# Kernel tuning notes

Hardware: AMD Instinct MI355X
Metric: run time of the kernel (lower is better)

## Reference

```python
import jax, jax.numpy as jnp
import numpy as np

B, D_IN, D, H, HD, M = 4096, 512, 128, 8, 16, 128
L = M + 1            # 1 query token + M memory slots
D_FF = 512
SCALE = 0.25         # 1/sqrt(HD)


def _ln(x, w, b, eps=1e-5):
    m = jnp.mean(x, axis=-1, keepdims=True)
    v = jnp.var(x, axis=-1, keepdims=True)
    return (x - m) * jax.lax.rsqrt(v + eps) * w + b


def setup_inputs() -> dict:
    ks = jax.random.split(jax.random.key(0), 26)
    n = lambda i, shape, s=1.0: jax.random.normal(ks[i], shape, jnp.float32) * s
    return {
        "x": n(0, (B, 1, D_IN)),
        "W_in": n(1, (D, D_IN), 0.05),
        "b_in": n(2, (D,), 0.02),
        "pos": n(3, (B, 1, D), 0.02),
        "mask": jnp.zeros((B, M), jnp.float32),  # additive attention bias for memory slots
        "mem": n(5, (B, M, D)),
        "ln1_w": jnp.ones((D,), jnp.float32), "ln1_b": jnp.zeros((D,), jnp.float32),
        "W_qkv": n(8, (3 * D, D), 0.09),
        "b_qkv": n(9, (3 * D,), 0.02),
        "W_out": n(10, (D, D), 0.09),
        "b_out": n(11, (D,), 0.02),
        "ln2_w": jnp.ones((D,), jnp.float32), "ln2_b": jnp.zeros((D,), jnp.float32),
        "ln3_w": jnp.ones((D,), jnp.float32), "ln3_b": jnp.zeros((D,), jnp.float32),
        "W_ff1": n(16, (D_FF, D), 0.09),
        "b_ff1": n(17, (D_FF,), 0.02),
        "ln4_w": jnp.ones((D_FF,), jnp.float32), "ln4_b": jnp.zeros((D_FF,), jnp.float32),
        "W_ff2": n(20, (D, D_FF), 0.04),
        "b_ff2": n(21, (D,), 0.02),
        "ln5_w": jnp.ones((D,), jnp.float32), "ln5_b": jnp.zeros((D,), jnp.float32),
        "W_head": n(24, (D_IN, D), 0.09),
        "b_head": n(25, (D_IN,), 0.02),
    }


def reference(x, W_in, b_in, pos, mask, mem, ln1_w, ln1_b, W_qkv, b_qkv,
              W_out, b_out, ln2_w, ln2_b, ln3_w, ln3_b, W_ff1, b_ff1,
              ln4_w, ln4_b, W_ff2, b_ff2, ln5_w, ln5_b, W_head, b_head):
    Bn = x.shape[0]
    # input projection + positional offset -> single query token per row  [B,1,D]
    q_in = (x.reshape(Bn, D_IN) @ W_in.T + b_in)[:, None, :] + pos
    # additive attention bias: 0 for the query slot, `mask` for memory slots  [B,L]
    bias = jnp.concatenate([jnp.zeros((Bn, 1), x.dtype), mask], axis=1)
    kv_in = jnp.concatenate([q_in, mem], axis=1)           # [B,L,D]
    kv_ln = _ln(kv_in, ln1_w, ln1_b)
    Wq, Wkv = W_qkv[:D], W_qkv[D:]
    bq, bkv = b_qkv[:D], b_qkv[D:]
    q = q_in[:, 0] @ Wq.T + bq                             # [B,D]  (Q uses UN-normalized q_in)
    kv = kv_ln @ Wkv.T + bkv                               # [B,L,2D]
    k, v = kv[..., :D], kv[..., D:]
    qh = q.reshape(Bn, H, HD)
    kh = k.reshape(Bn, L, H, HD)
    vh = v.reshape(Bn, L, H, HD)
    scores = jnp.einsum('bhd,blhd->bhl', qh * SCALE, kh) + bias[:, None, :]
    p = jax.nn.softmax(scores, axis=-1)                    # [B,H,L]
    o = jnp.einsum('bhl,blhd->bhd', p, vh).reshape(Bn, D)
    attn = _ln((o @ W_out.T + b_out)[:, None, :], ln2_w, ln2_b)
    h = attn + q_in                                        # residual  [B,1,D]
    f = _ln(h, ln3_w, ln3_b) @ W_ff1.T + b_ff1             # [B,1,D_FF]
    f = 0.5 * f * (1.0 + jax.lax.erf(f * 0.7071067811865476))  # exact GELU
    f = _ln(f, ln4_w, ln4_b) @ W_ff2.T + b_ff2             # [B,1,D]
    h2 = _ln(f + h, ln5_w, ln5_b)
    return h2 @ W_head.T + b_head                          # [B,1,D_IN]
```

## Files before the change

### kernel.cpp

```cpp
#include <hip/hip_runtime.h>

namespace {

constexpr int Dn   = 128;
constexpr int DIN  = 512;
constexpr int Hn   = 8;
constexpr int Mn   = 128;
constexpr int DFF  = 512;
constexpr int GA   = 4;
constexpr int GC   = 8;
constexpr float ATT_SCALE = 0.25f;
constexpr float INV_SQRT2 = 0.70710678118654752440f;

typedef short  short8v  __attribute__((ext_vector_type(8)));
typedef float  float4v  __attribute__((ext_vector_type(4)));

__device__ __forceinline__ unsigned pk_bf16(float lo, float hi) {
    unsigned r;
    asm volatile("v_cvt_pk_bf16_f32 %0, %1, %2" : "=v"(r) : "v"(lo), "v"(hi));
    return r;
}
__device__ __forceinline__ float lo16(unsigned u) { return __uint_as_float(u << 16); }
__device__ __forceinline__ float hi16(unsigned u) { return __uint_as_float(u & 0xffff0000u); }

__device__ __forceinline__ float dot128(const float* __restrict__ wrow,
                                        const float* __restrict__ v)
{
    const float4* w4 = (const float4*)wrow;
    const float4* v4 = (const float4*)v;
    float acc = 0.f;
#pragma unroll
    for (int j = 0; j < 32; ++j) {
        float4 a = w4[j], b = v4[j];
        acc += a.x*b.x + a.y*b.y + a.z*b.z + a.w*b.w;
    }
    return acc;
}

template <int NCOL>
__device__ __forceinline__ void ln_row64(const float* __restrict__ src,
                                         float* __restrict__ dst,
                                         const float* __restrict__ gw,
                                         const float* __restrict__ gb,
                                         const float* __restrict__ resid,
                                         int sub)
{
    constexpr int E = NCOL / 64;
    float v0[E]; float sm = 0.f;
#pragma unroll
    for (int i = 0; i < E; ++i) { v0[i] = src[sub*E + i]; sm += v0[i]; }
#pragma unroll
    for (int m = 32; m >= 1; m >>= 1) sm += __shfl_xor(sm, m);
    float mean = sm * (1.f / (float)NCOL);
    float vs = 0.f;
#pragma unroll
    for (int i = 0; i < E; ++i) { float d0 = v0[i] - mean; vs += d0*d0; }
#pragma unroll
    for (int m = 32; m >= 1; m >>= 1) vs += __shfl_xor(vs, m);
    float rstd = rsqrtf(vs * (1.f / (float)NCOL) + 1e-5f);
#pragma unroll
    for (int i = 0; i < E; ++i) {
        int d = sub*E + i;
        float r = (v0[i] - mean) * rstd * gw[d] + gb[d];
        dst[d] = resid ? (r + resid[d]) : r;
    }
}

__global__ __launch_bounds__(256, 2)
void k_qin(const float* __restrict__ x, const float* __restrict__ W_in,
           const float* __restrict__ b_in, const float* __restrict__ pos,
           float* __restrict__ q_in)
{
    const int t  = threadIdx.x;
    const int b0 = blockIdx.x * 8;
    __shared__ __align__(16) float s_x[8 * DIN];
    {
        const float4* src = (const float4*)(x + (size_t)b0 * DIN);
        float4* dst = (float4*)s_x;
#pragma unroll
        for (int i = 0; i < 4; ++i) dst[t + 256*i] = src[t + 256*i];
    }
    __syncthreads();
    {
        int d = t & 127, gq = t >> 7;
        const float4* w4 = (const float4*)(W_in + (size_t)d * DIN);
        float acc[4] = {0,0,0,0};
        for (int j = 0; j < DIN/4; ++j) {
            float4 a = w4[j];
#pragma unroll
            for (int g = 0; g < 4; ++g) {
                float4 xv = ((const float4*)s_x)[(gq*4 + g)*(DIN/4) + j];
                acc[g] = fmaf(a.x, xv.x, acc[g]); acc[g] = fmaf(a.y, xv.y, acc[g]);
                acc[g] = fmaf(a.z, xv.z, acc[g]); acc[g] = fmaf(a.w, xv.w, acc[g]);
            }
        }
#pragma unroll
        for (int g = 0; g < 4; ++g) {
            int gb = b0 + gq*4 + g;
            q_in[(size_t)gb*Dn + d] = acc[g] + b_in[d] + pos[(size_t)gb*Dn + d];
        }
    }
}

__global__ __launch_bounds__(256, 2)
void k_attn(const float* __restrict__ q_in,
            const float* __restrict__ mask,
            const float* __restrict__ mem,
            const float* __restrict__ ln1_w, const float* __restrict__ ln1_b,
            const float* __restrict__ W_qkv, const float* __restrict__ b_qkv,
            float* __restrict__ o_ws)
{
    const int t    = threadIdx.x;
    const int lane = t & 63;
    const int wv   = t >> 6;
    const int b0   = blockIdx.x * GA;

    __shared__ __align__(16) unsigned short s16[2][Mn * Dn];
    __shared__ __align__(16) float s_X[1312];
    __shared__ __align__(16) float s_lnq[Dn];
    __shared__ __align__(16) float s_q[Dn];
    __shared__ __align__(16) float s_qin[GA][Dn];
    __shared__ float s_s2c[Hn], s_s0[Hn], s_den[Hn], s_p0[Hn];

    unsigned short* s_At = (unsigned short*)s_X;
    float* s_sc = s_X;

    float4 pr[16];
    {
        const float4* src = (const float4*)(mem + (size_t)b0 * Mn * Dn);
#pragma unroll
        for (int i = 0; i < 16; ++i) pr[i] = src[t + 256*i];
    }
    if (t < 128)
        ((float4*)&s_qin[0][0])[t] = ((const float4*)(q_in + (size_t)b0*Dn))[t];
    __syncthreads();

    for (int g = 0; g < GA; ++g) {
        const int p = g & 1;

#pragma unroll
        for (int i = 0; i < 16; ++i) {
            int fid = t + 256*i;
            int r = fid >> 5, k = fid & 31;
            int c = k >> 1, half = k & 1;
            unsigned u0 = pk_bf16(pr[i].x, pr[i].y), u1 = pk_bf16(pr[i].z, pr[i].w);
            *(uint2*)&s16[p][r*128 + ((c ^ (r & 7)) << 3) + half*4] = make_uint2(u0, u1);
        }
        if (g + 1 < GA) {
            const float4* src = (const float4*)(mem + (size_t)(b0+g+1) * Mn * Dn);
#pragma unroll
            for (int i = 0; i < 16; ++i) pr[i] = src[t + 256*i];
        }
        if (t < 64) {
            ln_row64<Dn>(&s_qin[g][0], s_lnq, ln1_w, ln1_b, nullptr, t);
        } else if (t >= 128) {
            int dd = t - 128;
            s_q[dd] = dot128(W_qkv + (size_t)dd*Dn, &s_qin[g][0]) + b_qkv[dd];
        }
        __syncthreads();

        {
            int h = t >> 5, js = t & 31;
            float aq[4] = {0,0,0,0};
            float ch = 0.f;
#pragma unroll
            for (int d0 = 0; d0 < 16; ++d0) {
                float qv = s_q[h*16 + d0];
                float4 w = ((const float4*)(W_qkv + (size_t)(Dn + h*16 + d0)*Dn))[js];
                aq[0] = fmaf(qv, w.x, aq[0]); aq[1] = fmaf(qv, w.y, aq[1]);
                aq[2] = fmaf(qv, w.z, aq[2]); aq[3] = fmaf(qv, w.w, aq[3]);
                ch = fmaf(qv, b_qkv[Dn + h*16 + d0], ch);
            }
            ch *= ATT_SCALE;
            float s1p = 0.f, s2p = 0.f, s0p = 0.f;
            float aqw[4];
#pragma unroll
            for (int c = 0; c < 4; ++c) {
                int j = js*4 + c;
                float a = ATT_SCALE * aq[c];
                aqw[c] = a * ln1_w[j];
                s1p += aqw[c];
                s2p = fmaf(a, ln1_b[j], s2p);
                s0p = fmaf(a, s_lnq[j], s0p);
            }
#pragma unroll
            for (int m = 16; m >= 1; m >>= 1) {
                s1p += __shfl_xor(s1p, m, 32);
                s2p += __shfl_xor(s2p, m, 32);
                s0p += __shfl_xor(s0p, m, 32);
            }
            float sub = s1p * (1.f/128.f);
            *(unsigned*)&s_At[h*136 + 4*js]     = pk_bf16(aqw[0]-sub, aqw[1]-sub);
            *(unsigned*)&s_At[h*136 + 4*js + 2] = pk_bf16(aqw[2]-sub, aqw[3]-sub);
            if (js == 0) { s_s2c[h] = s2p + ch; s_s0[h] = s0p + ch; }
            unsigned* X32 = (unsigned*)s_At;
            for (int idx = t; idx < 544; idx += 256) X32[8*68 + idx] = 0;
        }
        __syncthreads();

        float4v acc0 = {0.f,0.f,0.f,0.f}, acc1 = {0.f,0.f,0.f,0.f};
        float rstd_reg = 0.f;
        {
            const int al = lane & 15, ag = lane >> 4;
            const int r0 = (2*wv)*16 + al, r1 = (2*wv+1)*16 + al;
#pragma unroll
            for (int ks = 0; ks < 4; ++ks) {
                short8v af = *(const short8v*)&s_At[al*136 + ks*32 + ag*8];
                int c = ks*4 + ag;
                short8v f0 = *(const short8v*)&s16[p][r0*128 + ((c ^ (r0 & 7)) << 3)];
                short8v f1 = *(const short8v*)&s16[p][r1*128 + ((c ^ (r1 & 7)) << 3)];
                acc0 = __builtin_amdgcn_mfma_f32_16x16x32_bf16(af, f0, acc0, 0, 0, 0);
                acc1 = __builtin_amdgcn_mfma_f32_16x16x32_bf16(af, f1, acc1, 0, 0, 0);
            }
            int r = t >> 1, hf = t & 1;
            float sum = 0.f, ssq = 0.f;
#pragma unroll
            for (int kk = 0; kk < 8; ++kk) {
                int c = hf*8 + kk;
                uint4 tv = *(const uint4*)&s16[p][r*128 + ((c ^ (r & 7)) << 3)];
                float vv[8];
                vv[0] = lo16(tv.x); vv[1] = hi16(tv.x);
                vv[2] = lo16(tv.y); vv[3] = hi16(tv.y);
                vv[4] = lo16(tv.z); vv[5] = hi16(tv.z);
                vv[6] = lo16(tv.w); vv[7] = hi16(tv.w);
#pragma unroll
                for (int q = 0; q < 8; ++q) { sum += vv[q]; ssq = fmaf(vv[q], vv[q], ssq); }
            }
            sum += __shfl_xor(sum, 1);
            ssq += __shfl_xor(ssq, 1);
            float mean = sum * (1.f/128.f);
            float var  = fmaf(-mean, mean, ssq * (1.f/128.f));
            rstd_reg = rsqrtf(var + 1e-5f);
        }
        __syncthreads();

        {
            if (lane < 32) {
                int al = lane & 15, hb = (lane >> 4) * 4;
                int r0 = (2*wv)*16 + al, r1 = (2*wv+1)*16 + al;
#pragma unroll
                for (int reg = 0; reg < 4; ++reg) {
                    s_sc[r0*10 + hb + reg] = acc0[reg];
                    s_sc[r1*10 + hb + reg] = acc1[reg];
                }
            }
            if ((t & 1) == 0) s_sc[(t >> 1)*10 + 8] = rstd_reg;
        }
        __syncthreads();

        {
            int w = wv, l = lane;
            int h0 = 2*w, h1 = h0 + 1;
            int r0 = 2*l, r1 = r0 + 1;
            float2 da = *(const float2*)&s_sc[r0*10 + h0];
            float2 db = *(const float2*)&s_sc[r1*10 + h0];
            float rs0 = s_sc[r0*10 + 8], rs1 = s_sc[r1*10 + 8];
            float2 mk = *(const float2*)&mask[(size_t)(b0+g)*Mn + r0];
            float sc00 = fmaf(rs0, da.x, s_s2c[h0]) + mk.x;
            float sc01 = fmaf(rs0, da.y, s_s2c[h1]) + mk.x;
            float sc10 = fmaf(rs1, db.x, s_s2c[h0]) + mk.y;
            float sc11 = fmaf(rs1, db.y, s_s2c[h1]) + mk.y;
            float mx0 = fmaxf(sc00, sc10), mx1 = fmaxf(sc01, sc11);
#pragma unroll
            for (int m = 1; m < 64; m <<= 1) {
                mx0 = fmaxf(mx0, __shfl_xor(mx0, m));
                mx1 = fmaxf(mx1, __shfl_xor(mx1, m));
            }
            mx0 = fmaxf(mx0, s_s0[h0]);
            mx1 = fmaxf(mx1, s_s0[h1]);
            float e00 = __expf(sc00 - mx0), e10 = __expf(sc10 - mx0);
            float e01 = __expf(sc01 - mx1), e11 = __expf(sc11 - mx1);
            float ds0 = e00 + e10, ds1 = e01 + e11;
#pragma unroll
            for (int m = 1; m < 64; m <<= 1) {
                ds0 += __shfl_xor(ds0, m);
                ds1 += __shfl_xor(ds1, m);
            }
            float p00 = __expf(s_s0[h0] - mx0), p01 = __expf(s_s0[h1] - mx1);
            *(float2*)&s_sc[r0*10 + h0] = make_float2(e00*rs0, e01*rs0);
            *(float2*)&s_sc[r1*10 + h0] = make_float2(e10*rs1, e11*rs1);
            if (l == 0) {
                s_den[h0] = ds0 + p00; s_p0[h0] = p00;
                s_den[h1] = ds1 + p01; s_p0[h1] = p01;
            }
        }
        __syncthreads();

        float cx0[8], cx1[8], cS0, cS1;
        {
            int w = wv, l = lane;
            int qtr = l >> 4, c = l & 15;
#pragma unroll
            for (int q = 0; q < 8; ++q) { cx0[q] = 0.f; cx1[q] = 0.f; }
#pragma unroll 4
            for (int rr = 0; rr < 32; ++rr) {
                int r = qtr*32 + rr;
                uint4 tv = *(const uint4*)&s16[p][r*128 + ((c ^ (r & 7)) << 3)];
                float2 qv = *(const float2*)&s_sc[r*10 + 2*w];
                float v0 = lo16(tv.x), v1 = hi16(tv.x);
                float v2 = lo16(tv.y), v3 = hi16(tv.y);
                float v4 = lo16(tv.z), v5 = hi16(tv.z);
                float v6 = lo16(tv.w), v7 = hi16(tv.w);
                cx0[0]=fmaf(qv.x,v0,cx0[0]); cx1[0]=fmaf(qv.y,v0,cx1[0]);
                cx0[1]=fmaf(qv.x,v1,cx0[1]); cx1[1]=fmaf(qv.y,v1,cx1[1]);
                cx0[2]=fmaf(qv.x,v2,cx0[2]); cx1[2]=fmaf(qv.y,v2,cx1[2]);
                cx0[3]=fmaf(qv.x,v3,cx0[3]); cx1[3]=fmaf(qv.y,v3,cx1[3]);
                cx0[4]=fmaf(qv.x,v4,cx0[4]); cx1[4]=fmaf(qv.y,v4,cx1[4]);
                cx0[5]=fmaf(qv.x,v5,cx0[5]); cx1[5]=fmaf(qv.y,v5,cx1[5]);
                cx0[6]=fmaf(qv.x,v6,cx0[6]); cx1[6]=fmaf(qv.y,v6,cx1[6]);
                cx0[7]=fmaf(qv.x,v7,cx0[7]); cx1[7]=fmaf(qv.y,v7,cx1[7]);
            }
#pragma unroll
            for (int q = 0; q < 8; ++q) {
                cx0[q] += __shfl_xor(cx0[q], 16);
                cx0[q] += __shfl_xor(cx0[q], 32);
                cx1[q] += __shfl_xor(cx1[q], 16);
                cx1[q] += __shfl_xor(cx1[q], 32);
            }
            float sA = ((cx0[0]+cx0[1])+(cx0[2]+cx0[3])) + ((cx0[4]+cx0[5])+(cx0[6]+cx0[7]));
            float sB = ((cx1[0]+cx1[1])+(cx1[2]+cx1[3])) + ((cx1[4]+cx1[5])+(cx1[6]+cx1[7]));
#pragma unroll
            for (int m = 1; m < 16; m <<= 1) {
                sA += __shfl_xor(sA, m);
                sB += __shfl_xor(sB, m);
            }
            cS0 = sA * (1.f/128.f);
            cS1 = sB * (1.f/128.f);
        }
        __syncthreads();

        if (lane < 16) {
            int c = lane;
            int h0 = 2*wv, h1 = h0 + 1;
            float den0 = s_den[h0], p0a = s_p0[h0], sP0 = den0 - p0a, inv0 = 1.f/den0;
            float den1 = s_den[h1], p0b = s_p0[h1], sP1 = den1 - p0b, inv1 = 1.f/den1;
#pragma unroll
            for (int q = 0; q < 2; ++q) {
                int j0 = c*8 + q*4;
                float4 lq = *(const float4*)&s_lnq[j0];
                float4 lw = *(const float4*)&ln1_w[j0];
                float4 lb = *(const float4*)&ln1_b[j0];
                float4 o0, o1;
                o0.x = (p0a*lq.x + lw.x*(cx0[q*4+0]-cS0) + lb.x*sP0) * inv0;
                o0.y = (p0a*lq.y + lw.y*(cx0[q*4+1]-cS0) + lb.y*sP0) * inv0;
                o0.z = (p0a*lq.z + lw.z*(cx0[q*4+2]-cS0) + lb.z*sP0) * inv0;
                o0.w = (p0a*lq.w + lw.w*(cx0[q*4+3]-cS0) + lb.w*sP0) * inv0;
                o1.x = (p0b*lq.x + lw.x*(cx1[q*4+0]-cS1) + lb.x*sP1) * inv1;
                o1.y = (p0b*lq.y + lw.y*(cx1[q*4+1]-cS1) + lb.y*sP1) * inv1;
                o1.z = (p0b*lq.z + lw.z*(cx1[q*4+2]-cS1) + lb.z*sP1) * inv1;
                o1.w = (p0b*lq.w + lw.w*(cx1[q*4+3]-cS1) + lb.w*sP1) * inv1;
                *(float4*)&s_X[h0*128 + j0] = o0;
                *(float4*)&s_X[h1*128 + j0] = o1;
            }
        }
        __syncthreads();

        {
            int d = t >> 1, half = t & 1;
            int h = d >> 4;
            const float4* w4 = (const float4*)(W_qkv + (size_t)(2*Dn + d)*Dn) + half*16;
            const float4* c4 = (const float4*)&s_X[h*128] + half*16;
            float acc = 0.f;
#pragma unroll
            for (int j = 0; j < 16; ++j) {
                float4 a = w4[j], v = c4[j];
                acc += a.x*v.x + a.y*v.y + a.z*v.z + a.w*v.w;
            }
            acc += __shfl_xor(acc, 1);
            if (half == 0)
                o_ws[(size_t)(b0+g)*Dn + d] = acc + b_qkv[2*Dn + d];
        }
        __syncthreads();
    }
}

__global__ __launch_bounds__(256, 2)
void k_tail(const float* __restrict__ q_in, const float* __restrict__ o_ws,
            const float* __restrict__ W_out, const float* __restrict__ b_out,
            const float* __restrict__ ln2_w, const float* __restrict__ ln2_b,
            const float* __restrict__ ln3_w, const float* __restrict__ ln3_b,
            const float* __restrict__ W_ff1, const float* __restrict__ b_ff1,
            const float* __restrict__ ln4_w, const float* __restrict__ ln4_b,
            const float* __restrict__ W_ff2, const float* __restrict__ b_ff2,
            const float* __restrict__ ln5_w, const float* __restrict__ ln5_b,
            const float* __restrict__ W_head, const float* __restrict__ b_head,
            float* __restrict__ out)
{
    const int t    = threadIdx.x;
    const int lane = t & 63;
    const int wv   = t >> 6;
    const int b0   = blockIdx.x * GC;

    __shared__ __align__(16) float s_qi[GC][Dn];
    __shared__ __align__(16) float s_o [GC][Dn];
    __shared__ __align__(16) float s_t1[GC][Dn];
    __shared__ __align__(16) float s_h [GC][Dn];
    __shared__ __align__(16) float s_l3[GC][Dn];
    __shared__ __align__(16) float s_f1[GC * DFF];

    ((float4*)&s_qi[0][0])[t] = ((const float4*)(q_in + (size_t)b0*Dn))[t];
    ((float4*)&s_o [0][0])[t] = ((const float4*)(o_ws + (size_t)b0*Dn))[t];
    __syncthreads();

    {
        int d = t & 127, grp = t >> 7;
        const float4* w4 = (const float4*)(W_out + (size_t)d * Dn);
        float acc[4] = {0,0,0,0};
#pragma unroll 8
        for (int j = 0; j < 32; ++j) {
            float4 a = w4[j];
#pragma unroll
            for (int gg = 0; gg < 4; ++gg) {
                float4 v = *(const float4*)&s_o[grp*4 + gg][j*4];
                acc[gg] = fmaf(a.x,v.x,acc[gg]); acc[gg] = fmaf(a.y,v.y,acc[gg]);
                acc[gg] = fmaf(a.z,v.z,acc[gg]); acc[gg] = fmaf(a.w,v.w,acc[gg]);
            }
        }
#pragma unroll
        for (int gg = 0; gg < 4; ++gg) s_t1[grp*4 + gg][d] = acc[gg] + b_out[d];
    }
    __syncthreads();

    ln_row64<Dn>(&s_t1[wv][0], &s_h[wv][0], ln2_w, ln2_b, &s_qi[wv][0], lane);
    ln_row64<Dn>(&s_t1[wv+4][0], &s_h[wv+4][0], ln2_w, ln2_b, &s_qi[wv+4][0], lane);
    __syncthreads();
    ln_row64<Dn>(&s_h[wv][0], &s_l3[wv][0], ln3_w, ln3_b, nullptr, lane);
    ln_row64<Dn>(&s_h[wv+4][0], &s_l3[wv+4][0], ln3_w, ln3_b, nullptr, lane);
    __syncthreads();

    {
        int e0 = t, e1 = t + 256;
        const float4* wa = (const float4*)(W_ff1 + (size_t)e0 * Dn);
        const float4* wb = (const float4*)(W_ff1 + (size_t)e1 * Dn);
        float acc0[GC], acc1[GC];
#pragma unroll
        for (int g = 0; g < GC; ++g) { acc0[g] = 0.f; acc1[g] = 0.f; }
#pragma unroll 2
        for (int j = 0; j < 32; ++j) {
            float4 a = wa[j], bb = wb[j];
#pragma unroll
            for (int g = 0; g < GC; ++g) {
                float4 v = *(const float4*)&s_l3[g][j*4];
                acc0[g] = fmaf(a.x,v.x,acc0[g]);  acc0[g] = fmaf(a.y,v.y,acc0[g]);
                acc0[g] = fmaf(a.z,v.z,acc0[g]);  acc0[g] = fmaf(a.w,v.w,acc0[g]);
                acc1[g] = fmaf(bb.x,v.x,acc1[g]); acc1[g] = fmaf(bb.y,v.y,acc1[g]);
                acc1[g] = fmaf(bb.z,v.z,acc1[g]); acc1[g] = fmaf(bb.w,v.w,acc1[g]);
            }
        }
#pragma unroll
        for (int g = 0; g < GC; ++g) {
            float v0 = acc0[g] + b_ff1[e0];
            float v1 = acc1[g] + b_ff1[e1];
            s_f1[g*DFF + e0] = 0.5f * v0 * (1.f + erff(v0 * INV_SQRT2));
            s_f1[g*DFF + e1] = 0.5f * v1 * (1.f + erff(v1 * INV_SQRT2));
        }
    }
    __syncthreads();

    ln_row64<DFF>(&s_f1[wv*DFF], &s_f1[wv*DFF], ln4_w, ln4_b, nullptr, lane);
    ln_row64<DFF>(&s_f1[(wv+4)*DFF], &s_f1[(wv+4)*DFF], ln4_w, ln4_b, nullptr, lane);
    __syncthreads();

    {
        int d = t & 127, grp = t >> 7;
        const float4* w4 = (const float4*)(W_ff2 + (size_t)d * DFF);
        float acc[4] = {0,0,0,0};
#pragma unroll 4
        for (int j = 0; j < DFF/4; ++j) {
            float4 a = w4[j];
#pragma unroll
            for (int gg = 0; gg < 4; ++gg) {
                float4 v = ((const float4*)&s_f1[(grp*4 + gg)*DFF])[j];
                acc[gg] = fmaf(a.x,v.x,acc[gg]); acc[gg] = fmaf(a.y,v.y,acc[gg]);
                acc[gg] = fmaf(a.z,v.z,acc[gg]); acc[gg] = fmaf(a.w,v.w,acc[gg]);
            }
        }
#pragma unroll
        for (int gg = 0; gg < 4; ++gg)
            s_t1[grp*4 + gg][d] = acc[gg] + b_ff2[d] + s_h[grp*4 + gg][d];
    }
    __syncthreads();

    ln_row64<Dn>(&s_t1[wv][0], &s_o[wv][0], ln5_w, ln5_b, nullptr, lane);
    ln_row64<Dn>(&s_t1[wv+4][0], &s_o[wv+4][0], ln5_w, ln5_b, nullptr, lane);
    __syncthreads();

    {
        int e0 = t, e1 = t + 256;
        const float4* wa = (const float4*)(W_head + (size_t)e0 * Dn);
        const float4* wb = (const float4*)(W_head + (size_t)e1 * Dn);
        float acc0[GC], acc1[GC];
#pragma unroll
        for (int g = 0; g < GC; ++g) { acc0[g] = 0.f; acc1[g] = 0.f; }
#pragma unroll 2
        for (int j = 0; j < 32; ++j) {
            float4 a = wa[j], bb = wb[j];
#pragma unroll
            for (int g = 0; g < GC; ++g) {
                float4 v = *(const float4*)&s_o[g][j*4];
                acc0[g] = fmaf(a.x,v.x,acc0[g]);  acc0[g] = fmaf(a.y,v.y,acc0[g]);
                acc0[g] = fmaf(a.z,v.z,acc0[g]);  acc0[g] = fmaf(a.w,v.w,acc0[g]);
                acc1[g] = fmaf(bb.x,v.x,acc1[g]); acc1[g] = fmaf(bb.y,v.y,acc1[g]);
                acc1[g] = fmaf(bb.z,v.z,acc1[g]); acc1[g] = fmaf(bb.w,v.w,acc1[g]);
            }
        }
#pragma unroll
        for (int g = 0; g < GC; ++g) {
            out[(size_t)(b0+g)*DIN + e0] = acc0[g] + b_head[e0];
            out[(size_t)(b0+g)*DIN + e1] = acc1[g] + b_head[e1];
        }
    }
}

}

extern "C" void kernel_launch(void* const* d_in, const int* in_sizes, int n_in,
                              void* d_out, int out_size, void* d_ws, size_t ws_size,
                              hipStream_t stream)
{
    const float* x      = (const float*)d_in[0];
    const float* W_in   = (const float*)d_in[1];
    const float* b_in   = (const float*)d_in[2];
    const float* pos    = (const float*)d_in[3];
    const float* mask   = (const float*)d_in[4];
    const float* mem    = (const float*)d_in[5];
    const float* ln1_w  = (const float*)d_in[6];
    const float* ln1_b  = (const float*)d_in[7];
    const float* W_qkv  = (const float*)d_in[8];
    const float* b_qkv  = (const float*)d_in[9];
    const float* W_out  = (const float*)d_in[10];
    const float* b_out  = (const float*)d_in[11];
    const float* ln2_w  = (const float*)d_in[12];
    const float* ln2_b  = (const float*)d_in[13];
    const float* ln3_w  = (const float*)d_in[14];
    const float* ln3_b  = (const float*)d_in[15];
    const float* W_ff1  = (const float*)d_in[16];
    const float* b_ff1  = (const float*)d_in[17];
    const float* ln4_w  = (const float*)d_in[18];
    const float* ln4_b  = (const float*)d_in[19];
    const float* W_ff2  = (const float*)d_in[20];
    const float* b_ff2  = (const float*)d_in[21];
    const float* ln5_w  = (const float*)d_in[22];
    const float* ln5_b  = (const float*)d_in[23];
    const float* W_head = (const float*)d_in[24];
    const float* b_head = (const float*)d_in[25];

    const int B = in_sizes[0] / DIN;
    float* ws_qin = (float*)d_ws;
    float* ws_o   = (float*)d_ws + (size_t)B * Dn;

    k_qin<<<dim3(B / 8), dim3(256), 0, stream>>>(x, W_in, b_in, pos, ws_qin);
    k_attn<<<dim3(B / GA), dim3(256), 0, stream>>>(ws_qin, mask, mem,
                                                   ln1_w, ln1_b, W_qkv, b_qkv, ws_o);
    k_tail<<<dim3(B / GC), dim3(256), 0, stream>>>(ws_qin, ws_o,
        W_out, b_out, ln2_w, ln2_b, ln3_w, ln3_b,
        W_ff1, b_ff1, ln4_w, ln4_b, W_ff2, b_ff2,
        ln5_w, ln5_b, W_head, b_head, (float*)d_out);
}
```

Baseline: 268.5 us.

## Process one batch row per attention block instead of register-prefetched groups of four

The attention kernel now launches one block per batch row rather than looping over four rows per block with a register prefetch of the next row's memory tile and double-buffered bf16 shared memory. This halves shared memory per block and frees the 64 prefetch registers, so more blocks can be resident and the hardware overlaps memory loads across blocks instead of within one. In exchange, each block loses software pipelining and re-reads the W_qkv weights for every row, and launches four times as many blocks.

Measured after the change: 254.3 us. -5.3%, faster.

```diff
diff --git a/kernel.cpp b/kernel.cpp
--- a/kernel.cpp
+++ b/kernel.cpp
@@ -7,7 +7,6 @@
 constexpr int Hn   = 8;
 constexpr int Mn   = 128;
 constexpr int DFF  = 512;
-constexpr int GA   = 4;
 constexpr int GC   = 8;
 constexpr float ATT_SCALE = 0.25f;
 constexpr float INV_SQRT2 = 0.70710678118654752440f;
@@ -113,264 +112,251 @@
     const int t    = threadIdx.x;
     const int lane = t & 63;
     const int wv   = t >> 6;
-    const int b0   = blockIdx.x * GA;
-
-    __shared__ __align__(16) unsigned short s16[2][Mn * Dn];
+    const int b    = blockIdx.x;
+
+    __shared__ __align__(16) unsigned short s16[Mn * Dn];
     __shared__ __align__(16) float s_X[1312];
     __shared__ __align__(16) float s_lnq[Dn];
+    __shared__ __align__(16) float s_qi[Dn];
     __shared__ __align__(16) float s_q[Dn];
-    __shared__ __align__(16) float s_qin[GA][Dn];
     __shared__ float s_s2c[Hn], s_s0[Hn], s_den[Hn], s_p0[Hn];
 
     unsigned short* s_At = (unsigned short*)s_X;
     float* s_sc = s_X;
 
-    float4 pr[16];
-    {
-        const float4* src = (const float4*)(mem + (size_t)b0 * Mn * Dn);
-#pragma unroll
-        for (int i = 0; i < 16; ++i) pr[i] = src[t + 256*i];
-    }
-    if (t < 128)
-        ((float4*)&s_qin[0][0])[t] = ((const float4*)(q_in + (size_t)b0*Dn))[t];
-    __syncthreads();
-
-    for (int g = 0; g < GA; ++g) {
-        const int p = g & 1;
-
+    if (t < 32) ((float4*)s_qi)[t] = ((const float4*)(q_in + (size_t)b*Dn))[t];
+    __syncthreads();
+
+    {
+        const float4* src = (const float4*)(mem + (size_t)b * Mn * Dn);
 #pragma unroll
         for (int i = 0; i < 16; ++i) {
             int fid = t + 256*i;
+            float4 v = src[fid];
             int r = fid >> 5, k = fid & 31;
             int c = k >> 1, half = k & 1;
-            unsigned u0 = pk_bf16(pr[i].x, pr[i].y), u1 = pk_bf16(pr[i].z, pr[i].w);
-            *(uint2*)&s16[p][r*128 + ((c ^ (r & 7)) << 3) + half*4] = make_uint2(u0, u1);
-        }
-        if (g + 1 < GA) {
-            const float4* src = (const float4*)(mem + (size_t)(b0+g+1) * Mn * Dn);
-#pragma unroll
-            for (int i = 0; i < 16; ++i) pr[i] = src[t + 256*i];
-        }
-        if (t < 64) {
-            ln_row64<Dn>(&s_qin[g][0], s_lnq, ln1_w, ln1_b, nullptr, t);
-        } else if (t >= 128) {
-            int dd = t - 128;
-            s_q[dd] = dot128(W_qkv + (size_t)dd*Dn, &s_qin[g][0]) + b_qkv[dd];
-        }
-        __syncthreads();
-
-        {
-            int h = t >> 5, js = t & 31;
-            float aq[4] = {0,0,0,0};
-            float ch = 0.f;
-#pragma unroll
-            for (int d0 = 0; d0 < 16; ++d0) {
-                float qv = s_q[h*16 + d0];
-                float4 w = ((const float4*)(W_qkv + (size_t)(Dn + h*16 + d0)*Dn))[js];
-                aq[0] = fmaf(qv, w.x, aq[0]); aq[1] = fmaf(qv, w.y, aq[1]);
-                aq[2] = fmaf(qv, w.z, aq[2]); aq[3] = fmaf(qv, w.w, aq[3]);
-                ch = fmaf(qv, b_qkv[Dn + h*16 + d0], ch);
+            unsigned u0 = pk_bf16(v.x, v.y), u1 = pk_bf16(v.z, v.w);
+            *(uint2*)&s16[r*128 + ((c ^ (r & 7)) << 3) + half*4] = make_uint2(u0, u1);
+        }
+    }
+    if (t < 64) {
+        ln_row64<Dn>(s_qi, s_lnq, ln1_w, ln1_b, nullptr, t);
+    } else if (t >= 128) {
+        int dd = t - 128;
+        s_q[dd] = dot128(W_qkv + (size_t)dd*Dn, s_qi) + b_qkv[dd];
+    }
+    __syncthreads();
+
+    {
+        int h = t >> 5, js = t & 31;
+        float aq[4] = {0,0,0,0};
+        float ch = 0.f;
+#pragma unroll
+        for (int d0 = 0; d0 < 16; ++d0) {
+            float qv = s_q[h*16 + d0];
+            float4 w = ((const float4*)(W_qkv + (size_t)(Dn + h*16 + d0)*Dn))[js];
+            aq[0] = fmaf(qv, w.x, aq[0]); aq[1] = fmaf(qv, w.y, aq[1]);
+            aq[2] = fmaf(qv, w.z, aq[2]); aq[3] = fmaf(qv, w.w, aq[3]);
+            ch = fmaf(qv, b_qkv[Dn + h*16 + d0], ch);
+        }
+        ch *= ATT_SCALE;
+        float s1p = 0.f, s2p = 0.f, s0p = 0.f;
+        float aqw[4];
+#pragma unroll
+        for (int c = 0; c < 4; ++c) {
+            int j = js*4 + c;
+            float a = ATT_SCALE * aq[c];
+            aqw[c] = a * ln1_w[j];
+            s1p += aqw[c];
+            s2p = fmaf(a, ln1_b[j], s2p);
+            s0p = fmaf(a, s_lnq[j], s0p);
+        }
+#pragma unroll
+        for (int m = 16; m >= 1; m >>= 1) {
+            s1p += __shfl_xor(s1p, m, 32);
+            s2p += __shfl_xor(s2p, m, 32);
+            s0p += __shfl_xor(s0p, m, 32);
+        }
+        float sub = s1p * (1.f/128.f);
+        *(unsigned*)&s_At[h*136 + 4*js]     = pk_bf16(aqw[0]-sub, aqw[1]-sub);
+        *(unsigned*)&s_At[h*136 + 4*js + 2] = pk_bf16(aqw[2]-sub, aqw[3]-sub);
+        if (js == 0) { s_s2c[h] = s2p + ch; s_s0[h] = s0p + ch; }
+        unsigned* X32 = (unsigned*)s_At;
+        for (int idx = t; idx < 544; idx += 256) X32[8*68 + idx] = 0;
+    }
+    __syncthreads();
+
+    float4v acc0 = {0.f,0.f,0.f,0.f}, acc1 = {0.f,0.f,0.f,0.f};
+    float rstd_reg = 0.f;
+    {
+        const int al = lane & 15, ag = lane >> 4;
+        const int r0 = (2*wv)*16 + al, r1 = (2*wv+1)*16 + al;
+#pragma unroll
+        for (int ks = 0; ks < 4; ++ks) {
+            short8v af = *(const short8v*)&s_At[al*136 + ks*32 + ag*8];
+            int c = ks*4 + ag;
+            short8v b0 = *(const short8v*)&s16[r0*128 + ((c ^ (r0 & 7)) << 3)];
+            short8v b1 = *(const short8v*)&s16[r1*128 + ((c ^ (r1 & 7)) << 3)];
+            acc0 = __builtin_amdgcn_mfma_f32_16x16x32_bf16(af, b0, acc0, 0, 0, 0);
+            acc1 = __builtin_amdgcn_mfma_f32_16x16x32_bf16(af, b1, acc1, 0, 0, 0);
+        }
+        int r = t >> 1, hf = t & 1;
+        float sum = 0.f, ssq = 0.f;
+#pragma unroll
+        for (int kk = 0; kk < 8; ++kk) {
+            int c = hf*8 + kk;
+            uint4 tv = *(const uint4*)&s16[r*128 + ((c ^ (r & 7)) << 3)];
+            float vv[8];
+            vv[0] = lo16(tv.x); vv[1] = hi16(tv.x);
+            vv[2] = lo16(tv.y); vv[3] = hi16(tv.y);
+            vv[4] = lo16(tv.z); vv[5] = hi16(tv.z);
+            vv[6] = lo16(tv.w); vv[7] = hi16(tv.w);
+#pragma unroll
+            for (int q = 0; q < 8; ++q) { sum += vv[q]; ssq = fmaf(vv[q], vv[q], ssq); }
+        }
+        sum += __shfl_xor(sum, 1);
+        ssq += __shfl_xor(ssq, 1);
+        float mean = sum * (1.f/128.f);
+        float var  = fmaf(-mean, mean, ssq * (1.f/128.f));
+        rstd_reg = rsqrtf(var + 1e-5f);
+    }
+    __syncthreads();
+
+    {
+        if (lane < 32) {
+            int al = lane & 15, hb = (lane >> 4) * 4;
+            int r0 = (2*wv)*16 + al, r1 = (2*wv+1)*16 + al;
+#pragma unroll
+            for (int reg = 0; reg < 4; ++reg) {
+                s_sc[r0*10 + hb + reg] = acc0[reg];
+                s_sc[r1*10 + hb + reg] = acc1[reg];
             }
-            ch *= ATT_SCALE;
-            float s1p = 0.f, s2p = 0.f, s0p = 0.f;
-            float aqw[4];
-#pragma unroll
-            for (int c = 0; c < 4; ++c) {
-                int j = js*4 + c;
-                float a = ATT_SCALE * aq[c];
-                aqw[c] = a * ln1_w[j];
-                s1p += aqw[c];
-                s2p = fmaf(a, ln1_b[j], s2p);
-                s0p = fmaf(a, s_lnq[j], s0p);
-            }
-#pragma unroll
-            for (int m = 16; m >= 1; m >>= 1) {
-                s1p += __shfl_xor(s1p, m, 32);
-                s2p += __shfl_xor(s2p, m, 32);
-                s0p += __shfl_xor(s0p, m, 32);
-            }
-            float sub = s1p * (1.f/128.f);
-            *(unsigned*)&s_At[h*136 + 4*js]     = pk_bf16(aqw[0]-sub, aqw[1]-sub);
-            *(unsigned*)&s_At[h*136 + 4*js + 2] = pk_bf16(aqw[2]-sub, aqw[3]-sub);
-            if (js == 0) { s_s2c[h] = s2p + ch; s_s0[h] = s0p + ch; }
-            unsigned* X32 = (unsigned*)s_At;
-            for (int idx = t; idx < 544; idx += 256) X32[8*68 + idx] = 0;
-        }
-        __syncthreads();
-
-        float4v acc0 = {0.f,0.f,0.f,0.f}, acc1 = {0.f,0.f,0.f,0.f};
-        float rstd_reg = 0.f;
-        {
-            const int al = lane & 15, ag = lane >> 4;
-            const int r0 = (2*wv)*16 + al, r1 = (2*wv+1)*16 + al;
-#pragma unroll
-            for (int ks = 0; ks < 4; ++ks) {
-                short8v af = *(const short8v*)&s_At[al*136 + ks*32 + ag*8];
-                int c = ks*4 + ag;
-                short8v f0 = *(const short8v*)&s16[p][r0*128 + ((c ^ (r0 & 7)) << 3)];
-                short8v f1 = *(const short8v*)&s16[p][r1*128 + ((c ^ (r1 & 7)) << 3)];
-                acc0 = __builtin_amdgcn_mfma_f32_16x16x32_bf16(af, f0, acc0, 0, 0, 0);
-                acc1 = __builtin_amdgcn_mfma_f32_16x16x32_bf16(af, f1, acc1, 0, 0, 0);
-            }
-            int r = t >> 1, hf = t & 1;
-            float sum = 0.f, ssq = 0.f;
-#pragma unroll
-            for (int kk = 0; kk < 8; ++kk) {
-                int c = hf*8 + kk;
-                uint4 tv = *(const uint4*)&s16[p][r*128 + ((c ^ (r & 7)) << 3)];
-                float vv[8];
-                vv[0] = lo16(tv.x); vv[1] = hi16(tv.x);
-                vv[2] = lo16(tv.y); vv[3] = hi16(tv.y);
-                vv[4] = lo16(tv.z); vv[5] = hi16(tv.z);
-                vv[6] = lo16(tv.w); vv[7] = hi16(tv.w);
-#pragma unroll
-                for (int q = 0; q < 8; ++q) { sum += vv[q]; ssq = fmaf(vv[q], vv[q], ssq); }
-            }
-            sum += __shfl_xor(sum, 1);
-            ssq += __shfl_xor(ssq, 1);
-            float mean = sum * (1.f/128.f);
-            float var  = fmaf(-mean, mean, ssq * (1.f/128.f));
-            rstd_reg = rsqrtf(var + 1e-5f);
-        }
-        __syncthreads();
-
-        {
-            if (lane < 32) {
-                int al = lane & 15, hb = (lane >> 4) * 4;
-                int r0 = (2*wv)*16 + al, r1 = (2*wv+1)*16 + al;
-#pragma unroll
-                for (int reg = 0; reg < 4; ++reg) {
-                    s_sc[r0*10 + hb + reg] = acc0[reg];
-                    s_sc[r1*10 + hb + reg] = acc1[reg];
-                }
-            }
-            if ((t & 1) == 0) s_sc[(t >> 1)*10 + 8] = rstd_reg;
-        }
-        __syncthreads();
-
-        {
-            int w = wv, l = lane;
-            int h0 = 2*w, h1 = h0 + 1;
-            int r0 = 2*l, r1 = r0 + 1;
-            float2 da = *(const float2*)&s_sc[r0*10 + h0];
-            float2 db = *(const float2*)&s_sc[r1*10 + h0];
-            float rs0 = s_sc[r0*10 + 8], rs1 = s_sc[r1*10 + 8];
-            float2 mk = *(const float2*)&mask[(size_t)(b0+g)*Mn + r0];
-            float sc00 = fmaf(rs0, da.x, s_s2c[h0]) + mk.x;
-            float sc01 = fmaf(rs0, da.y, s_s2c[h1]) + mk.x;
-            float sc10 = fmaf(rs1, db.x, s_s2c[h0]) + mk.y;
-            float sc11 = fmaf(rs1, db.y, s_s2c[h1]) + mk.y;
-            float mx0 = fmaxf(sc00, sc10), mx1 = fmaxf(sc01, sc11);
-#pragma unroll
-            for (int m = 1; m < 64; m <<= 1) {
-                mx0 = fmaxf(mx0, __shfl_xor(mx0, m));
-                mx1 = fmaxf(mx1, __shfl_xor(mx1, m));
-            }
-            mx0 = fmaxf(mx0, s_s0[h0]);
-            mx1 = fmaxf(mx1, s_s0[h1]);
-            float e00 = __expf(sc00 - mx0), e10 = __expf(sc10 - mx0);
-            float e01 = __expf(sc01 - mx1), e11 = __expf(sc11 - mx1);
-            float ds0 = e00 + e10, ds1 = e01 + e11;
-#pragma unroll
-            for (int m = 1; m < 64; m <<= 1) {
-                ds0 += __shfl_xor(ds0, m);
-                ds1 += __shfl_xor(ds1, m);
-            }
-            float p00 = __expf(s_s0[h0] - mx0), p01 = __expf(s_s0[h1] - mx1);
-            *(float2*)&s_sc[r0*10 + h0] = make_float2(e00*rs0, e01*rs0);
-            *(float2*)&s_sc[r1*10 + h0] = make_float2(e10*rs1, e11*rs1);
-            if (l == 0) {
-                s_den[h0] = ds0 + p00; s_p0[h0] = p00;
-                s_den[h1] = ds1 + p01; s_p0[h1] = p01;
-            }
-        }
-        __syncthreads();
-
-        float cx0[8], cx1[8], cS0, cS1;
-        {
-            int w = wv, l = lane;
-            int qtr = l >> 4, c = l & 15;
-#pragma unroll
-            for (int q = 0; q < 8; ++q) { cx0[q] = 0.f; cx1[q] = 0.f; }
+        }
+        if ((t & 1) == 0) s_sc[(t >> 1)*10 + 8] = rstd_reg;
+    }
+    __syncthreads();
+
+    {
+        int w = wv, l = lane;
+        int h0 = 2*w, h1 = h0 + 1;
+        int r0 = 2*l, r1 = r0 + 1;
+        float2 da = *(const float2*)&s_sc[r0*10 + h0];
+        float2 db = *(const float2*)&s_sc[r1*10 + h0];
+        float rs0 = s_sc[r0*10 + 8], rs1 = s_sc[r1*10 + 8];
+        float2 mk = *(const float2*)&mask[(size_t)b*Mn + r0];
+        float sc00 = fmaf(rs0, da.x, s_s2c[h0]) + mk.x;
+        float sc01 = fmaf(rs0, da.y, s_s2c[h1]) + mk.x;
+        float sc10 = fmaf(rs1, db.x, s_s2c[h0]) + mk.y;
+        float sc11 = fmaf(rs1, db.y, s_s2c[h1]) + mk.y;
+        float mx0 = fmaxf(sc00, sc10), mx1 = fmaxf(sc01, sc11);
+#pragma unroll
+        for (int m = 1; m < 64; m <<= 1) {
+            mx0 = fmaxf(mx0, __shfl_xor(mx0, m));
+            mx1 = fmaxf(mx1, __shfl_xor(mx1, m));
+        }
+        mx0 = fmaxf(mx0, s_s0[h0]);
+        mx1 = fmaxf(mx1, s_s0[h1]);
+        float e00 = __expf(sc00 - mx0), e10 = __expf(sc10 - mx0);
+        float e01 = __expf(sc01 - mx1), e11 = __expf(sc11 - mx1);
+        float ds0 = e00 + e10, ds1 = e01 + e11;
+#pragma unroll
+        for (int m = 1; m < 64; m <<= 1) {
+            ds0 += __shfl_xor(ds0, m);
+            ds1 += __shfl_xor(ds1, m);
+        }
+        float p00 = __expf(s_s0[h0] - mx0), p01 = __expf(s_s0[h1] - mx1);
+        *(float2*)&s_sc[r0*10 + h0] = make_float2(e00*rs0, e01*rs0);
+        *(float2*)&s_sc[r1*10 + h0] = make_float2(e10*rs1, e11*rs1);
+        if (l == 0) {
+            s_den[h0] = ds0 + p00; s_p0[h0] = p00;
+            s_den[h1] = ds1 + p01; s_p0[h1] = p01;
+        }
+    }
+    __syncthreads();
+
+    float cx0[8], cx1[8], cS0, cS1;
+    {
+        int w = wv, l = lane;
+        int qtr = l >> 4, c = l & 15;
+#pragma unroll
+        for (int q = 0; q < 8; ++q) { cx0[q] = 0.f; cx1[q] = 0.f; }
 #pragma unroll 4
-            for (int rr = 0; rr < 32; ++rr) {
-                int r = qtr*32 + rr;
-                uint4 tv = *(const uint4*)&s16[p][r*128 + ((c ^ (r & 7)) << 3)];
-                float2 qv = *(const float2*)&s_sc[r*10 + 2*w];
-                float v0 = lo16(tv.x), v1 = hi16(tv.x);
-                float v2 = lo16(tv.y), v3 = hi16(tv.y);
-                float v4 = lo16(tv.z), v5 = hi16(tv.z);
-                float v6 = lo16(tv.w), v7 = hi16(tv.w);
-                cx0[0]=fmaf(qv.x,v0,cx0[0]); cx1[0]=fmaf(qv.y,v0,cx1[0]);
-                cx0[1]=fmaf(qv.x,v1,cx0[1]); cx1[1]=fmaf(qv.y,v1,cx1[1]);
-                cx0[2]=fmaf(qv.x,v2,cx0[2]); cx1[2]=fmaf(qv.y,v2,cx1[2]);
-                cx0[3]=fmaf(qv.x,v3,cx0[3]); cx1[3]=fmaf(qv.y,v3,cx1[3]);
-                cx0[4]=fmaf(qv.x,v4,cx0[4]); cx1[4]=fmaf(qv.y,v4,cx1[4]);
-                cx0[5]=fmaf(qv.x,v5,cx0[5]); cx1[5]=fmaf(qv.y,v5,cx1[5]);
-                cx0[6]=fmaf(qv.x,v6,cx0[6]); cx1[6]=fmaf(qv.y,v6,cx1[6]);
-                cx0[7]=fmaf(qv.x,v7,cx0[7]); cx1[7]=fmaf(qv.y,v7,cx1[7]);
-            }
-#pragma unroll
-            for (int q = 0; q < 8; ++q) {
-                cx0[q] += __shfl_xor(cx0[q], 16);
-                cx0[q] += __shfl_xor(cx0[q], 32);
-                cx1[q] += __shfl_xor(cx1[q], 16);
-                cx1[q] += __shfl_xor(cx1[q], 32);
-            }
-            float sA = ((cx0[0]+cx0[1])+(cx0[2]+cx0[3])) + ((cx0[4]+cx0[5])+(cx0[6]+cx0[7]));
-            float sB = ((cx1[0]+cx1[1])+(cx1[2]+cx1[3])) + ((cx1[4]+cx1[5])+(cx1[6]+cx1[7]));
-#pragma unroll
-            for (int m = 1; m < 16; m <<= 1) {
-                sA += __shfl_xor(sA, m);
-                sB += __shfl_xor(sB, m);
-            }
-            cS0 = sA * (1.f/128.f);
-            cS1 = sB * (1.f/128.f);
-        }
-        __syncthreads();
-
-        if (lane < 16) {
-            int c = lane;
-            int h0 = 2*wv, h1 = h0 + 1;
-            float den0 = s_den[h0], p0a = s_p0[h0], sP0 = den0 - p0a, inv0 = 1.f/den0;
-            float den1 = s_den[h1], p0b = s_p0[h1], sP1 = den1 - p0b, inv1 = 1.f/den1;
-#pragma unroll
-            for (int q = 0; q < 2; ++q) {
-                int j0 = c*8 + q*4;
-                float4 lq = *(const float4*)&s_lnq[j0];
-                float4 lw = *(const float4*)&ln1_w[j0];
-                float4 lb = *(const float4*)&ln1_b[j0];
-                float4 o0, o1;
-                o0.x = (p0a*lq.x + lw.x*(cx0[q*4+0]-cS0) + lb.x*sP0) * inv0;
-                o0.y = (p0a*lq.y + lw.y*(cx0[q*4+1]-cS0) + lb.y*sP0) * inv0;
-                o0.z = (p0a*lq.z + lw.z*(cx0[q*4+2]-cS0) + lb.z*sP0) * inv0;
-                o0.w = (p0a*lq.w + lw.w*(cx0[q*4+3]-cS0) + lb.w*sP0) * inv0;
-                o1.x = (p0b*lq.x + lw.x*(cx1[q*4+0]-cS1) + lb.x*sP1) * inv1;
-                o1.y = (p0b*lq.y + lw.y*(cx1[q*4+1]-cS1) + lb.y*sP1) * inv1;
-                o1.z = (p0b*lq.z + lw.z*(cx1[q*4+2]-cS1) + lb.z*sP1) * inv1;
-                o1.w = (p0b*lq.w + lw.w*(cx1[q*4+3]-cS1) + lb.w*sP1) * inv1;
-                *(float4*)&s_X[h0*128 + j0] = o0;
-                *(float4*)&s_X[h1*128 + j0] = o1;
-            }
-        }
-        __syncthreads();
-
-        {
-            int d = t >> 1, half = t & 1;
-            int h = d >> 4;
-            const float4* w4 = (const float4*)(W_qkv + (size_t)(2*Dn + d)*Dn) + half*16;
-            const float4* c4 = (const float4*)&s_X[h*128] + half*16;
-            float acc = 0.f;
-#pragma unroll
-            for (int j = 0; j < 16; ++j) {
-                float4 a = w4[j], v = c4[j];
-                acc += a.x*v.x + a.y*v.y + a.z*v.z + a.w*v.w;
-            }
-            acc += __shfl_xor(acc, 1);
-            if (half == 0)
-                o_ws[(size_t)(b0+g)*Dn + d] = acc + b_qkv[2*Dn + d];
-        }
-        __syncthreads();
+        for (int rr = 0; rr < 32; ++rr) {
+            int r = qtr*32 + rr;
+            uint4 tv = *(const uint4*)&s16[r*128 + ((c ^ (r & 7)) << 3)];
+            float2 qv = *(const float2*)&s_sc[r*10 + 2*w];
+            float v0 = lo16(tv.x), v1 = hi16(tv.x);
+            float v2 = lo16(tv.y), v3 = hi16(tv.y);
+            float v4 = lo16(tv.z), v5 = hi16(tv.z);
+            float v6 = lo16(tv.w), v7 = hi16(tv.w);
+            cx0[0]=fmaf(qv.x,v0,cx0[0]); cx1[0]=fmaf(qv.y,v0,cx1[0]);
+            cx0[1]=fmaf(qv.x,v1,cx0[1]); cx1[1]=fmaf(qv.y,v1,cx1[1]);
+            cx0[2]=fmaf(qv.x,v2,cx0[2]); cx1[2]=fmaf(qv.y,v2,cx1[2]);
+            cx0[3]=fmaf(qv.x,v3,cx0[3]); cx1[3]=fmaf(qv.y,v3,cx1[3]);
+            cx0[4]=fmaf(qv.x,v4,cx0[4]); cx1[4]=fmaf(qv.y,v4,cx1[4]);
+            cx0[5]=fmaf(qv.x,v5,cx0[5]); cx1[5]=fmaf(qv.y,v5,cx1[5]);
+            cx0[6]=fmaf(qv.x,v6,cx0[6]); cx1[6]=fmaf(qv.y,v6,cx1[6]);
+            cx0[7]=fmaf(qv.x,v7,cx0[7]); cx1[7]=fmaf(qv.y,v7,cx1[7]);
+        }
+#pragma unroll
+        for (int q = 0; q < 8; ++q) {
+            cx0[q] += __shfl_xor(cx0[q], 16);
+            cx0[q] += __shfl_xor(cx0[q], 32);
+            cx1[q] += __shfl_xor(cx1[q], 16);
+            cx1[q] += __shfl_xor(cx1[q], 32);
+        }
+        float sA = ((cx0[0]+cx0[1])+(cx0[2]+cx0[3])) + ((cx0[4]+cx0[5])+(cx0[6]+cx0[7]));
+        float sB = ((cx1[0]+cx1[1])+(cx1[2]+cx1[3])) + ((cx1[4]+cx1[5])+(cx1[6]+cx1[7]));
+#pragma unroll
+        for (int m = 1; m < 16; m <<= 1) {
+            sA += __shfl_xor(sA, m);
+            sB += __shfl_xor(sB, m);
+        }
+        cS0 = sA * (1.f/128.f);
+        cS1 = sB * (1.f/128.f);
+    }
+    __syncthreads();
+
+    if (lane < 16) {
+        int c = lane;
+        int h0 = 2*wv, h1 = h0 + 1;
+        float den0 = s_den[h0], p0a = s_p0[h0], sP0 = den0 - p0a, inv0 = 1.f/den0;
+        float den1 = s_den[h1], p0b = s_p0[h1], sP1 = den1 - p0b, inv1 = 1.f/den1;
+#pragma unroll
+        for (int q = 0; q < 2; ++q) {
+            int j0 = c*8 + q*4;
+            float4 lq = *(const float4*)&s_lnq[j0];
+            float4 lw = *(const float4*)&ln1_w[j0];
+            float4 lb = *(const float4*)&ln1_b[j0];
+            float4 o0, o1;
+            o0.x = (p0a*lq.x + lw.x*(cx0[q*4+0]-cS0) + lb.x*sP0) * inv0;
+            o0.y = (p0a*lq.y + lw.y*(cx0[q*4+1]-cS0) + lb.y*sP0) * inv0;
+            o0.z = (p0a*lq.z + lw.z*(cx0[q*4+2]-cS0) + lb.z*sP0) * inv0;
+            o0.w = (p0a*lq.w + lw.w*(cx0[q*4+3]-cS0) + lb.w*sP0) * inv0;
+            o1.x = (p0b*lq.x + lw.x*(cx1[q*4+0]-cS1) + lb.x*sP1) * inv1;
+            o1.y = (p0b*lq.y + lw.y*(cx1[q*4+1]-cS1) + lb.y*sP1) * inv1;
+            o1.z = (p0b*lq.z + lw.z*(cx1[q*4+2]-cS1) + lb.z*sP1) * inv1;
+            o1.w = (p0b*lq.w + lw.w*(cx1[q*4+3]-cS1) + lb.w*sP1) * inv1;
+            *(float4*)&s_X[h0*128 + j0] = o0;
+            *(float4*)&s_X[h1*128 + j0] = o1;
+        }
+    }
+    __syncthreads();
+
+    {
+        int d = t >> 1, half = t & 1;
+        int h = d >> 4;
+        const float4* w4 = (const float4*)(W_qkv + (size_t)(2*Dn + d)*Dn) + half*16;
+        const float4* c4 = (const float4*)&s_X[h*128] + half*16;
+        float acc = 0.f;
+#pragma unroll
+        for (int j = 0; j < 16; ++j) {
+            float4 a = w4[j], v = c4[j];
+            acc += a.x*v.x + a.y*v.y + a.z*v.z + a.w*v.w;
+        }
+        acc += __shfl_xor(acc, 1);
+        if (half == 0)
+            o_ws[(size_t)b*Dn + d] = acc + b_qkv[2*Dn + d];
     }
 }
 
@@ -550,8 +536,8 @@
     float* ws_o   = (float*)d_ws + (size_t)B * Dn;
 
     k_qin<<<dim3(B / 8), dim3(256), 0, stream>>>(x, W_in, b_in, pos, ws_qin);
-    k_attn<<<dim3(B / GA), dim3(256), 0, stream>>>(ws_qin, mask, mem,
-                                                   ln1_w, ln1_b, W_qkv, b_qkv, ws_o);
+    k_attn<<<dim3(B), dim3(256), 0, stream>>>(ws_qin, mask, mem,
+                                              ln1_w, ln1_b, W_qkv, b_qkv, ws_o);
     k_tail<<<dim3(B / GC), dim3(256), 0, stream>>>(ws_qin, ws_o,
         W_out, b_out, ln2_w, ln2_b, ln3_w, ln3_b,
         W_ff1, b_ff1, ln4_w, ln4_b, W_ff2, b_ff2,
```
